# Kernel optimization log

Measured on AMD Instinct MI355X. Metric: run time of the kernel, lower is better.

The kernel has to match this reference:

```python
import jax, jax.numpy as jnp
import numpy as np

USER_NUM = 100000
ITEM_NUM = 100000
N_NODES = USER_NUM + ITEM_NUM
EMB = 64
NNZ = 4000000
N_LAYERS = 3


def setup_inputs() -> dict:
    key = jax.random.key(0)
    k1, k2, k3, k4, k5 = jax.random.split(key, 5)
    # xavier-ish init for embeddings
    scale = np.sqrt(6.0 / (USER_NUM + EMB)).astype(np.float32)
    user_emb = jax.random.uniform(k1, (USER_NUM, EMB), jnp.float32, -scale, scale)
    item_emb = jax.random.uniform(k2, (ITEM_NUM, EMB), jnp.float32, -scale, scale)
    # COO sparse normalized adjacency: values ~ 1/deg scale
    adj_row = jax.random.randint(k3, (NNZ,), 0, N_NODES, dtype=jnp.int64)
    adj_col = jax.random.randint(k4, (NNZ,), 0, N_NODES, dtype=jnp.int64)
    adj_val = jax.random.uniform(k5, (NNZ,), jnp.float32) * (1.0 / 20.0)
    return {"user_emb": user_emb, "item_emb": item_emb,
            "adj_row": adj_row, "adj_col": adj_col, "adj_val": adj_val}


def _spmm(adj_row, adj_col, adj_val, x):
    # y[r] = sum_{e: row[e]==r} val[e] * x[col[e]]   (COO SpMM)
    msg = adj_val[:, None] * x[adj_col]  # [nnz, EMB]
    return jax.ops.segment_sum(msg, adj_row, num_segments=N_NODES)


def reference(user_emb, item_emb, adj_row, adj_col, adj_val):
    ego = jnp.concatenate([user_emb, item_emb], axis=0)  # [N, EMB]
    acc = jnp.zeros_like(ego)
    for _ in range(N_LAYERS):
        ego = _spmm(adj_row, adj_col, adj_val, ego)
        acc = acc + ego
    final = acc / N_LAYERS  # mean over stacked layer outputs
    return final[:USER_NUM], final[USER_NUM:]
```

## Files before the change

### kernel.cpp

```cpp
#include <hip/hip_runtime.h>
#include <hip/hip_fp16.h>

#define EMB 64
#define BROWS 128
#define BSHIFT 7
#define LDSN 2048
#define CHUNK 16384
#define CAP 3072

typedef int   iv4 __attribute__((ext_vector_type(4)));
typedef float fv4 __attribute__((ext_vector_type(4)));
typedef unsigned uv2 __attribute__((ext_vector_type(2)));

__global__ __launch_bounds__(1024) void fused_scatter(
        const int* __restrict__ rows, const int* __restrict__ cols,
        const float* __restrict__ vals, int* __restrict__ cursor,
        int2* __restrict__ packed, int nnz, int nbuck) {
    __shared__ int lc[LDSN];
    __shared__ int lbase[LDSN];
    int base = blockIdx.x * CHUNK;
    int end  = min(base + CHUNK, nnz);
    for (int i = threadIdx.x; i < LDSN; i += 1024) lc[i] = 0;
    __syncthreads();
    int nfull = (end - base) & ~3;
    for (int i = base + threadIdx.x * 4; i < base + nfull; i += 4096) {
        iv4 r = *(const iv4*)(rows + i);
        atomicAdd(&lc[r.x >> BSHIFT], 1);
        atomicAdd(&lc[r.y >> BSHIFT], 1);
        atomicAdd(&lc[r.z >> BSHIFT], 1);
        atomicAdd(&lc[r.w >> BSHIFT], 1);
    }
    {
        int t = base + nfull + threadIdx.x;
        if (t < end) atomicAdd(&lc[rows[t] >> BSHIFT], 1);
    }
    __syncthreads();
    for (int i = threadIdx.x; i < nbuck; i += 1024) {
        int v = lc[i];
        lbase[i] = i * CAP + (v ? atomicAdd(&cursor[i], v) : 0);
        lc[i] = 0;
    }
    __syncthreads();
    for (int i = base + threadIdx.x * 4; i < base + nfull; i += 4096) {
        iv4 r = *(const iv4*)(rows + i);
        iv4 c = __builtin_nontemporal_load((const iv4*)(cols + i));
        fv4 v = __builtin_nontemporal_load((const fv4*)(vals + i));
        int bk0 = r.x >> BSHIFT, bk1 = r.y >> BSHIFT;
        int bk2 = r.z >> BSHIFT, bk3 = r.w >> BSHIFT;
        int s0 = lbase[bk0] + atomicAdd(&lc[bk0], 1);
        int s1 = lbase[bk1] + atomicAdd(&lc[bk1], 1);
        int s2 = lbase[bk2] + atomicAdd(&lc[bk2], 1);
        int s3 = lbase[bk3] + atomicAdd(&lc[bk3], 1);
        packed[s0] = make_int2(c.x | ((r.x & (BROWS - 1)) << 18), __float_as_int(v.x));
        packed[s1] = make_int2(c.y | ((r.y & (BROWS - 1)) << 18), __float_as_int(v.y));
        packed[s2] = make_int2(c.z | ((r.z & (BROWS - 1)) << 18), __float_as_int(v.z));
        packed[s3] = make_int2(c.w | ((r.w & (BROWS - 1)) << 18), __float_as_int(v.w));
    }
    {
        int t = base + nfull + threadIdx.x;
        if (t < end) {
            int r = rows[t];
            int bk = r >> BSHIFT;
            int slot = lbase[bk] + atomicAdd(&lc[bk], 1);
            packed[slot] = make_int2(cols[t] | ((r & (BROWS - 1)) << 18),
                                     __float_as_int(vals[t]));
        }
    }
}

__global__ __launch_bounds__(512) void sort_bucket(
        int2* __restrict__ packed, const int* __restrict__ cursor,
        int* __restrict__ offs, int* __restrict__ oend, int n_rows) {
    __shared__ int2 ebuf[CAP];
    __shared__ int cnt[BROWS];
    __shared__ int coff[BROWS];
    int b = blockIdx.x;
    int s = b * CAP;
    int sz = cursor[b];
    int tid = threadIdx.x;
    if (tid < BROWS) cnt[tid] = 0;
    __syncthreads();
    int npair = sz >> 1;
    for (int ip = tid; ip < npair; ip += 512) {
        iv4 two = *(const iv4*)(packed + s + ip * 2);
        ebuf[ip * 2]     = make_int2(two.x, two.y);
        ebuf[ip * 2 + 1] = make_int2(two.z, two.w);
        atomicAdd(&cnt[(two.x >> 18) & (BROWS - 1)], 1);
        atomicAdd(&cnt[(two.z >> 18) & (BROWS - 1)], 1);
    }
    if ((sz & 1) && tid == 0) {
        int2 ed = packed[s + sz - 1];
        ebuf[sz - 1] = ed;
        atomicAdd(&cnt[(ed.x >> 18) & (BROWS - 1)], 1);
    }
    __syncthreads();
    int v = (tid < BROWS) ? cnt[tid] : 0;
    if (tid < BROWS) coff[tid] = v;
    __syncthreads();
    for (int off = 1; off < BROWS; off <<= 1) {
        int add = (tid < BROWS && tid >= off) ? coff[tid - off] : 0;
        __syncthreads();
        if (tid < BROWS) coff[tid] += add;
        __syncthreads();
    }
    if (tid < BROWS) {
        int incl = coff[tid];
        int ex = incl - v;
        cnt[tid] = ex;
        int row = (b << BSHIFT) + tid;
        if (row < n_rows) { offs[row] = s + ex; oend[row] = s + incl; }
    }
    __syncthreads();
    for (int i = tid; i < sz; i += 512) {
        int2 ed = ebuf[i];
        int rl = (ed.x >> 18) & (BROWS - 1);
        int pos = atomicAdd(&cnt[rl], 1);
        packed[s + pos] = make_int2(ed.x & 0x3FFFF, ed.y);
    }
}

__global__ __launch_bounds__(256) void cast_concat_half(
        const float* __restrict__ a, const float* __restrict__ b,
        int na4, int ntot4, __half* __restrict__ o,
        int* __restrict__ cursor, int nbuck) {
    if (blockIdx.x == 0)
        for (int i = threadIdx.x; i < nbuck; i += 256) cursor[i] = 0;
    int stride = gridDim.x * blockDim.x;
    for (int i = blockIdx.x * blockDim.x + threadIdx.x; i < ntot4; i += stride) {
        fv4 v = (i < na4) ? ((const fv4*)a)[i] : ((const fv4*)b)[i - na4];
        __half2 h0 = __floats2half2_rn(v.x, v.y);
        __half2 h1 = __floats2half2_rn(v.z, v.w);
        uv2 w;
        w.x = *(unsigned*)&h0;
        w.y = *(unsigned*)&h1;
        *((uv2*)o + i) = w;
    }
}

__global__ __launch_bounds__(256) void spmm_row_h(
        const int* __restrict__ offs, const int* __restrict__ oend,
        const int2* __restrict__ packed, const __half* __restrict__ xh,
        __half* __restrict__ yh, const __half* __restrict__ ph,
        __half* __restrict__ pho, float* __restrict__ out, int n_rows, int mode) {
    int wid = (blockIdx.x * blockDim.x + threadIdx.x) >> 6;
    if (wid >= n_rows) return;
    int lane = threadIdx.x & 63;
    int r = __builtin_amdgcn_readfirstlane(wid);
    int s = offs[r];
    int e = oend[r];
    const unsigned long long* pk = (const unsigned long long*)packed;
    float a0 = 0.f, a1 = 0.f, a2 = 0.f, a3 = 0.f;
    float a4 = 0.f, a5 = 0.f, a6 = 0.f, a7 = 0.f;
    int k = s;
    for (; k + 15 < e; k += 16) {
        unsigned long long w0  = __builtin_nontemporal_load(pk + k);
        unsigned long long w1  = __builtin_nontemporal_load(pk + k + 1);
        unsigned long long w2  = __builtin_nontemporal_load(pk + k + 2);
        unsigned long long w3  = __builtin_nontemporal_load(pk + k + 3);
        unsigned long long w4  = __builtin_nontemporal_load(pk + k + 4);
        unsigned long long w5  = __builtin_nontemporal_load(pk + k + 5);
        unsigned long long w6  = __builtin_nontemporal_load(pk + k + 6);
        unsigned long long w7  = __builtin_nontemporal_load(pk + k + 7);
        unsigned long long w8  = __builtin_nontemporal_load(pk + k + 8);
        unsigned long long w9  = __builtin_nontemporal_load(pk + k + 9);
        unsigned long long w10 = __builtin_nontemporal_load(pk + k + 10);
        unsigned long long w11 = __builtin_nontemporal_load(pk + k + 11);
        unsigned long long w12 = __builtin_nontemporal_load(pk + k + 12);
        unsigned long long w13 = __builtin_nontemporal_load(pk + k + 13);
        unsigned long long w14 = __builtin_nontemporal_load(pk + k + 14);
        unsigned long long w15 = __builtin_nontemporal_load(pk + k + 15);
        float h0  = __half2float(xh[(((int)(unsigned)w0)  << 6) + lane]);
        float h1  = __half2float(xh[(((int)(unsigned)w1)  << 6) + lane]);
        float h2  = __half2float(xh[(((int)(unsigned)w2)  << 6) + lane]);
        float h3  = __half2float(xh[(((int)(unsigned)w3)  << 6) + lane]);
        float h4  = __half2float(xh[(((int)(unsigned)w4)  << 6) + lane]);
        float h5  = __half2float(xh[(((int)(unsigned)w5)  << 6) + lane]);
        float h6  = __half2float(xh[(((int)(unsigned)w6)  << 6) + lane]);
        float h7  = __half2float(xh[(((int)(unsigned)w7)  << 6) + lane]);
        float h8  = __half2float(xh[(((int)(unsigned)w8)  << 6) + lane]);
        float h9  = __half2float(xh[(((int)(unsigned)w9)  << 6) + lane]);
        float h10 = __half2float(xh[(((int)(unsigned)w10) << 6) + lane]);
        float h11 = __half2float(xh[(((int)(unsigned)w11) << 6) + lane]);
        float h12 = __half2float(xh[(((int)(unsigned)w12) << 6) + lane]);
        float h13 = __half2float(xh[(((int)(unsigned)w13) << 6) + lane]);
        float h14 = __half2float(xh[(((int)(unsigned)w14) << 6) + lane]);
        float h15 = __half2float(xh[(((int)(unsigned)w15) << 6) + lane]);
        a0 += __int_as_float((int)(w0  >> 32)) * h0;
        a1 += __int_as_float((int)(w1  >> 32)) * h1;
        a2 += __int_as_float((int)(w2  >> 32)) * h2;
        a3 += __int_as_float((int)(w3  >> 32)) * h3;
        a4 += __int_as_float((int)(w4  >> 32)) * h4;
        a5 += __int_as_float((int)(w5  >> 32)) * h5;
        a6 += __int_as_float((int)(w6  >> 32)) * h6;
        a7 += __int_as_float((int)(w7  >> 32)) * h7;
        a0 += __int_as_float((int)(w8  >> 32)) * h8;
        a1 += __int_as_float((int)(w9  >> 32)) * h9;
        a2 += __int_as_float((int)(w10 >> 32)) * h10;
        a3 += __int_as_float((int)(w11 >> 32)) * h11;
        a4 += __int_as_float((int)(w12 >> 32)) * h12;
        a5 += __int_as_float((int)(w13 >> 32)) * h13;
        a6 += __int_as_float((int)(w14 >> 32)) * h14;
        a7 += __int_as_float((int)(w15 >> 32)) * h15;
    }
    for (; k + 7 < e; k += 8) {
        unsigned long long w0 = __builtin_nontemporal_load(pk + k);
        unsigned long long w1 = __builtin_nontemporal_load(pk + k + 1);
        unsigned long long w2 = __builtin_nontemporal_load(pk + k + 2);
        unsigned long long w3 = __builtin_nontemporal_load(pk + k + 3);
        unsigned long long w4 = __builtin_nontemporal_load(pk + k + 4);
        unsigned long long w5 = __builtin_nontemporal_load(pk + k + 5);
        unsigned long long w6 = __builtin_nontemporal_load(pk + k + 6);
        unsigned long long w7 = __builtin_nontemporal_load(pk + k + 7);
        float h0 = __half2float(xh[(((int)(unsigned)w0) << 6) + lane]);
        float h1 = __half2float(xh[(((int)(unsigned)w1) << 6) + lane]);
        float h2 = __half2float(xh[(((int)(unsigned)w2) << 6) + lane]);
        float h3 = __half2float(xh[(((int)(unsigned)w3) << 6) + lane]);
        float h4 = __half2float(xh[(((int)(unsigned)w4) << 6) + lane]);
        float h5 = __half2float(xh[(((int)(unsigned)w5) << 6) + lane]);
        float h6 = __half2float(xh[(((int)(unsigned)w6) << 6) + lane]);
        float h7 = __half2float(xh[(((int)(unsigned)w7) << 6) + lane]);
        a0 += __int_as_float((int)(w0 >> 32)) * h0;
        a1 += __int_as_float((int)(w1 >> 32)) * h1;
        a2 += __int_as_float((int)(w2 >> 32)) * h2;
        a3 += __int_as_float((int)(w3 >> 32)) * h3;
        a4 += __int_as_float((int)(w4 >> 32)) * h4;
        a5 += __int_as_float((int)(w5 >> 32)) * h5;
        a6 += __int_as_float((int)(w6 >> 32)) * h6;
        a7 += __int_as_float((int)(w7 >> 32)) * h7;
    }
    for (; k + 3 < e; k += 4) {
        unsigned long long w0 = __builtin_nontemporal_load(pk + k);
        unsigned long long w1 = __builtin_nontemporal_load(pk + k + 1);
        unsigned long long w2 = __builtin_nontemporal_load(pk + k + 2);
        unsigned long long w3 = __builtin_nontemporal_load(pk + k + 3);
        float h0 = __half2float(xh[(((int)(unsigned)w0) << 6) + lane]);
        float h1 = __half2float(xh[(((int)(unsigned)w1) << 6) + lane]);
        float h2 = __half2float(xh[(((int)(unsigned)w2) << 6) + lane]);
        float h3 = __half2float(xh[(((int)(unsigned)w3) << 6) + lane]);
        a0 += __int_as_float((int)(w0 >> 32)) * h0;
        a1 += __int_as_float((int)(w1 >> 32)) * h1;
        a2 += __int_as_float((int)(w2 >> 32)) * h2;
        a3 += __int_as_float((int)(w3 >> 32)) * h3;
    }
    for (; k < e; ++k) {
        unsigned long long w = __builtin_nontemporal_load(pk + k);
        a0 += __int_as_float((int)(w >> 32)) *
              __half2float(xh[(((int)(unsigned)w) << 6) + lane]);
    }
    float acc = ((a0 + a1) + (a2 + a3)) + ((a4 + a5) + (a6 + a7));
    size_t oi = ((size_t)r << 6) + lane;
    if (mode == 0) {
        yh[oi] = __float2half_rn(acc);
    } else if (mode == 1) {
        float p = __half2float(ph[oi]);
        pho[oi] = __float2half_rn(p + acc);
        yh[oi] = __float2half_rn(acc);
    } else {
        float p = __half2float(ph[oi]);
        __builtin_nontemporal_store((p + acc) * (1.0f / 3.0f), &out[oi]);
    }
}

extern "C" void kernel_launch(void* const* d_in, const int* in_sizes, int n_in,
                              void* d_out, int out_size, void* d_ws, size_t ws_size,
                              hipStream_t stream) {
    const float* user_emb = (const float*)d_in[0];
    const float* item_emb = (const float*)d_in[1];
    const int*   adj_row  = (const int*)d_in[2];
    const int*   adj_col  = (const int*)d_in[3];
    const float* adj_val  = (const float*)d_in[4];
    float* out = (float*)d_out;

    const int n_user = in_sizes[0] / EMB;
    const int n_item = in_sizes[1] / EMB;
    const int n      = n_user + n_item;
    const int nnz    = in_sizes[2];
    const size_t half_bytes = (size_t)n * EMB * sizeof(__half);
    const int nbuck  = (n + BROWS - 1) >> BSHIFT;
    const int nchunk = (nnz + CHUNK - 1) / CHUNK;

    char* p = (char*)d_ws;
    __half* X0    = (__half*)p; p += half_bytes;
    __half* Ah    = (__half*)p; p += half_bytes;
    __half* Bh    = (__half*)p; p += half_bytes;
    int2*  packed = (int2*)p;  p += (size_t)nbuck * CAP * sizeof(int2);
    int*   offs   = (int*)p;   p += (size_t)n * sizeof(int);
    int*   oend   = (int*)p;   p += (size_t)n * sizeof(int);
    int*   cursor = (int*)p;   p += (size_t)nbuck * sizeof(int);

    cast_concat_half<<<2048, 256, 0, stream>>>(user_emb, item_emb,
                                               n_user * EMB / 4, n * EMB / 4, X0,
                                               cursor, nbuck);

    fused_scatter<<<nchunk, 1024, 0, stream>>>(adj_row, adj_col, adj_val,
                                               cursor, packed, nnz, nbuck);
    sort_bucket<<<nbuck, 512, 0, stream>>>(packed, cursor, offs, oend, n);

    const int sgrid = (n * EMB + 255) / 256;
    spmm_row_h<<<sgrid, 256, 0, stream>>>(offs, oend, packed, X0,
                                          Ah, Ah, Ah, out, n, 0);
    spmm_row_h<<<sgrid, 256, 0, stream>>>(offs, oend, packed, Ah,
                                          Bh, Ah, X0, out, n, 1);
    spmm_row_h<<<sgrid, 256, 0, stream>>>(offs, oend, packed, Bh,
                                          Bh, X0, Bh, out, n, 2);
}
```

Measured before the change: 487.3 us.

## Fuse embedding cast into scatter kernel and halve scatter chunk size

Moves the fp32-to-half cast and concat of the embeddings into extra blocks of the scatter kernel, so the cast runs alongside the bucket scatter and one launch is dropped. The cursor reset now uses hipMemsetAsync instead of being done inside the cast kernel. CHUNK is halved to 8192, doubling the number of scatter blocks for more parallelism, at the cost of more global cursor atomics and per-block LDS histogram overhead.

```diff
diff --git a/kernel.cpp b/kernel.cpp
--- a/kernel.cpp
+++ b/kernel.cpp
@@ -5,17 +5,33 @@
 #define BROWS 128
 #define BSHIFT 7
 #define LDSN 2048
-#define CHUNK 16384
+#define CHUNK 8192
 #define CAP 3072
+#define CASTB 512
 
 typedef int   iv4 __attribute__((ext_vector_type(4)));
 typedef float fv4 __attribute__((ext_vector_type(4)));
 typedef unsigned uv2 __attribute__((ext_vector_type(2)));
 
-__global__ __launch_bounds__(1024) void fused_scatter(
+__global__ __launch_bounds__(1024) void scatter_cast(
         const int* __restrict__ rows, const int* __restrict__ cols,
         const float* __restrict__ vals, int* __restrict__ cursor,
-        int2* __restrict__ packed, int nnz, int nbuck) {
+        int2* __restrict__ packed, int nnz, int nbuck, int nchunk,
+        const float* __restrict__ ua, const float* __restrict__ ib,
+        int na4, int ntot4, __half* __restrict__ xo) {
+    if (blockIdx.x >= nchunk) {
+        int stride = CASTB * 1024;
+        for (int i = (blockIdx.x - nchunk) * 1024 + threadIdx.x; i < ntot4; i += stride) {
+            fv4 v = (i < na4) ? ((const fv4*)ua)[i] : ((const fv4*)ib)[i - na4];
+            __half2 h0 = __floats2half2_rn(v.x, v.y);
+            __half2 h1 = __floats2half2_rn(v.z, v.w);
+            uv2 w;
+            w.x = *(unsigned*)&h0;
+            w.y = *(unsigned*)&h1;
+            *((uv2*)xo + i) = w;
+        }
+        return;
+    }
     __shared__ int lc[LDSN];
     __shared__ int lbase[LDSN];
     int base = blockIdx.x * CHUNK;
@@ -116,24 +132,6 @@
         int rl = (ed.x >> 18) & (BROWS - 1);
         int pos = atomicAdd(&cnt[rl], 1);
         packed[s + pos] = make_int2(ed.x & 0x3FFFF, ed.y);
-    }
-}
-
-__global__ __launch_bounds__(256) void cast_concat_half(
-        const float* __restrict__ a, const float* __restrict__ b,
-        int na4, int ntot4, __half* __restrict__ o,
-        int* __restrict__ cursor, int nbuck) {
-    if (blockIdx.x == 0)
-        for (int i = threadIdx.x; i < nbuck; i += 256) cursor[i] = 0;
-    int stride = gridDim.x * blockDim.x;
-    for (int i = blockIdx.x * blockDim.x + threadIdx.x; i < ntot4; i += stride) {
-        fv4 v = (i < na4) ? ((const fv4*)a)[i] : ((const fv4*)b)[i - na4];
-        __half2 h0 = __floats2half2_rn(v.x, v.y);
-        __half2 h1 = __floats2half2_rn(v.z, v.w);
-        uv2 w;
-        w.x = *(unsigned*)&h0;
-        w.y = *(unsigned*)&h1;
-        *((uv2*)o + i) = w;
     }
 }
 
@@ -288,12 +286,10 @@
     int*   oend   = (int*)p;   p += (size_t)n * sizeof(int);
     int*   cursor = (int*)p;   p += (size_t)nbuck * sizeof(int);
 
-    cast_concat_half<<<2048, 256, 0, stream>>>(user_emb, item_emb,
-                                               n_user * EMB / 4, n * EMB / 4, X0,
-                                               cursor, nbuck);
-
-    fused_scatter<<<nchunk, 1024, 0, stream>>>(adj_row, adj_col, adj_val,
-                                               cursor, packed, nnz, nbuck);
+    hipMemsetAsync(cursor, 0, (size_t)nbuck * sizeof(int), stream);
+    scatter_cast<<<nchunk + CASTB, 1024, 0, stream>>>(
+        adj_row, adj_col, adj_val, cursor, packed, nnz, nbuck, nchunk,
+        user_emb, item_emb, n_user * EMB / 4, n * EMB / 4, X0);
     sort_bucket<<<nbuck, 512, 0, stream>>>(packed, cursor, offs, oend, n);
 
     const int sgrid = (n * EMB + 255) / 256;
```

New measurement: 475.8 us. 1.02x faster.
